# Kernel optimization log

Measured on AMD Instinct MI355X. Metric: run time of the kernel, lower is better.

## Reference

```python
import jax, jax.numpy as jnp
import numpy as np
from jax import lax

B, T = 64, 200
NUM_C, DIM_S, SIZE_M = 2000, 128, 50


def setup_inputs() -> dict:
    key = jax.random.key(0)
    ks = jax.random.split(key, 12)
    d = {}
    d['skill'] = jax.random.randint(ks[0], (B, T), 0, NUM_C)
    d['answer'] = jax.random.randint(ks[1], (B, T), 0, 2)
    s = 1.0 / np.sqrt(DIM_S)
    d['k_emb'] = jax.random.normal(ks[2], (NUM_C + 1, DIM_S), jnp.float32)
    d['v_emb'] = jax.random.normal(ks[3], (2 * NUM_C + 1, DIM_S), jnp.float32)
    # kaiming_normal on [size_m, dim_s]: std = sqrt(2/dim_s)
    d['Mk'] = jax.random.normal(ks[4], (SIZE_M, DIM_S), jnp.float32) * np.sqrt(2.0 / DIM_S)
    d['Mv0'] = jax.random.normal(ks[5], (SIZE_M, DIM_S), jnp.float32) * np.sqrt(2.0 / DIM_S)
    d['f_W'] = jax.random.normal(ks[6], (DIM_S, 2 * DIM_S), jnp.float32) * (1.0 / np.sqrt(2 * DIM_S))
    d['f_b'] = jnp.zeros((DIM_S,), jnp.float32)
    d['p_W'] = jax.random.normal(ks[7], (NUM_C, DIM_S), jnp.float32) * s
    d['p_b'] = jnp.zeros((NUM_C,), jnp.float32)
    d['e_W'] = jax.random.normal(ks[8], (DIM_S, DIM_S), jnp.float32) * s
    d['e_b'] = jnp.zeros((DIM_S,), jnp.float32)
    d['a_W'] = jax.random.normal(ks[9], (DIM_S, DIM_S), jnp.float32) * s
    d['a_b'] = jnp.zeros((DIM_S,), jnp.float32)
    return d


def reference(skill, answer, k_emb, v_emb, Mk, Mv0, f_W, f_b, p_W, p_b, e_W, e_b, a_W, a_b):
    num_c = p_W.shape[0]
    bsz = skill.shape[0]
    answer_x = jnp.where(answer == 2, 1, answer)
    x = skill + num_c * answer_x                       # [B,T]
    k = k_emb[skill]                                   # [B,T,D]
    v = v_emb[x]                                       # [B,T,D]
    w = jax.nn.softmax(jnp.einsum('btd,md->btm', k, Mk), axis=-1)   # [B,T,M]
    e = jax.nn.sigmoid(jnp.einsum('btd,ed->bte', v, e_W) + e_b)      # [B,T,D]
    a = jnp.tanh(jnp.einsum('btd,ed->bte', v, a_W) + a_b)            # [B,T,D]

    Mv_init = jnp.broadcast_to(Mv0, (bsz,) + Mv0.shape)              # [B,M,D]

    def step(Mvt, inp):
        et, at, wt = inp                               # [B,D],[B,D],[B,M]
        # read uses pre-update memory (Mv[:, :-1] in the torch code)
        read = jnp.einsum('bm,bmd->bd', wt, Mvt)
        Mvt_new = Mvt * (1.0 - wt[:, :, None] * et[:, None, :]) + wt[:, :, None] * at[:, None, :]
        return Mvt_new, read

    _, reads = lax.scan(step, Mv_init,
                        (e.transpose(1, 0, 2), a.transpose(1, 0, 2), w.transpose(1, 0, 2)))
    reads = reads.transpose(1, 0, 2)                   # [B,T,D]

    f = jnp.tanh(jnp.concatenate([reads, k], axis=-1) @ f_W.T + f_b)  # [B,T,D]
    p = jax.nn.sigmoid(f @ p_W.T + p_b)                # [B,T,num_c] (dropout is identity at eval)
    p = p[:, :-1, :]
    next_skill = skill[:, 1:]                          # [B,T-1]
    idx = jnp.minimum(next_skill, num_c - 1)
    pred = jnp.take_along_axis(p, idx[..., None], axis=-1)[..., 0]
    pred = jnp.where(next_skill < num_c, pred, 0.0)    # index num_c -> zero row in torch one_hot
    return pred
```

## Files before the change

kernel.cpp:

```cpp
#include <hip/hip_runtime.h>
#include <math.h>

#define Bsz 64
#define Tn 200
#define NUMC 2000
#define DS 128
#define SM 50
#define NTOK (Bsz*Tn)
#define WG2 10
#define MPG2 5

typedef __attribute__((ext_vector_type(8))) short bfrag;
typedef __attribute__((ext_vector_type(4))) float f32x4;
typedef __attribute__((ext_vector_type(4))) unsigned int u32x4;

__device__ __forceinline__ unsigned short f2bf(float x) {
    unsigned int u = __builtin_bit_cast(unsigned int, x);
    u = u + 0x7fffu + ((u >> 16) & 1u);
    return (unsigned short)(u >> 16);
}
__device__ __forceinline__ unsigned int pack2(float a, float b) {
    return (unsigned int)f2bf(a) | ((unsigned int)f2bf(b) << 16);
}
__device__ __forceinline__ bfrag mk_frag(f32x4 x, f32x4 y) {
    u32x4 t;
    t[0] = pack2(x[0], x[1]); t[1] = pack2(x[2], x[3]);
    t[2] = pack2(y[0], y[1]); t[3] = pack2(y[2], y[3]);
    return __builtin_bit_cast(bfrag, t);
}

__device__ __forceinline__ float fast_exp(float x)  { return __builtin_amdgcn_exp2f(x * 1.44269504f); }
__device__ __forceinline__ float fast_rcp(float x)  { return __builtin_amdgcn_rcpf(x); }
__device__ __forceinline__ float fast_sigmoid(float x) { return fast_rcp(1.f + fast_exp(-x)); }
__device__ __forceinline__ float fast_tanh(float x) { return 1.f - 2.f * fast_rcp(fast_exp(2.f * x) + 1.f); }

__device__ __forceinline__ void load_group(const bfrag* __restrict__ B, int nt0, int L, bfrag bf[4][4]) {
    #pragma unroll
    for (int t = 0; t < 4; t++)
        #pragma unroll
        for (int ki = 0; ki < 4; ki++)
            bf[t][ki] = B[(size_t)((nt0 + t) * 4 + ki) * 64 + L];
}
__device__ __forceinline__ void mfma_group(const bfrag A[4], const bfrag bf[4][4], f32x4 acc[4]) {
    #pragma unroll
    for (int ki = 0; ki < 4; ki++)
        #pragma unroll
        for (int t = 0; t < 4; t++)
            acc[t] = __builtin_amdgcn_mfma_f32_16x16x32_bf16(A[ki], bf[t][ki], acc[t], 0, 0, 0);
}

__global__ __launch_bounds__(256) void k0_cast(
    const float* __restrict__ eW, const float* __restrict__ aW,
    const float* __restrict__ fW, const float* __restrict__ Mk,
    unsigned int* __restrict__ BeaU, unsigned int* __restrict__ BkmU,
    unsigned int* __restrict__ Bf0U)
{
    const int g = blockIdx.x * 256 + threadIdx.x;
    if (g >= 9216) return;
    int gm, mat;
    unsigned int* dst;
    if (g < 4096)      { mat = 0; gm = g;        dst = BeaU; }
    else if (g < 7168) { mat = 1; gm = g - 4096; dst = BkmU; }
    else               { mat = 2; gm = g - 7168; dst = Bf0U; }
    const int nt = gm >> 8, r = gm & 255, ki = r >> 6, L = r & 63;
    const int n = nt * 16 + (L & 15);
    const int k = ki * 32 + (L >> 4) * 8;

    const float* src = nullptr;
    if (mat == 0) {
        src = (n < 128) ? (eW + (size_t)n * DS + k) : (aW + (size_t)(n - 128) * DS + k);
    } else if (mat == 1) {
        if (n < 128)      src = fW + (size_t)n * (2 * DS) + DS + k;
        else if (n < 128 + SM) src = Mk + (size_t)(n - 128) * DS + k;
    } else {
        src = fW + (size_t)n * (2 * DS) + k;
    }
    float v[8];
    #pragma unroll
    for (int j = 0; j < 8; j++) v[j] = src ? src[j] : 0.f;
    u32x4 o;
    o[0] = pack2(v[0], v[1]); o[1] = pack2(v[2], v[3]);
    o[2] = pack2(v[4], v[5]); o[3] = pack2(v[6], v[7]);
    ((u32x4*)dst)[gm] = o;
}

__global__ __launch_bounds__(64) void k1_gemm(
    const int* __restrict__ skill, const int* __restrict__ answer,
    const float* __restrict__ k_emb, const float* __restrict__ v_emb,
    const unsigned int* __restrict__ BeaU, const unsigned int* __restrict__ BkmU,
    const float* __restrict__ eB, const float* __restrict__ aB,
    float* __restrict__ w_buf, float* __restrict__ e_buf,
    float* __restrict__ a_buf, float* __restrict__ kp_buf)
{
    const int bid = blockIdx.x;
    const int L = threadIdx.x, L15 = L & 15, quad = L >> 4;

    if (bid < NTOK/16) {
        const int tok0 = bid * 16;
        const int tokA = tok0 + L15;
        const int tokD0 = tok0 + quad * 4;

        const bfrag* Bea = (const bfrag*)BeaU;
        bfrag bfA[4][4], bfB[4][4];
        load_group(Bea, 0, L, bfA);
        load_group(Bea, 4, L, bfB);

        const int s  = skill[tokA];
        const int an = answer[tokA];
        const int ax = (an == 2) ? 1 : an;
        const float* vp = v_emb + ((size_t)(s + NUMC * ax)) * DS + quad * 8;
        bfrag Vf[4];
        #pragma unroll
        for (int ki = 0; ki < 4; ki++) {
            const f32x4* a = (const f32x4*)(vp + ki * 32);
            Vf[ki] = mk_frag(a[0], a[1]);
        }

        f32x4 acc[4];
        #pragma unroll
        for (int t = 0; t < 4; t++) acc[t] = (f32x4){0.f,0.f,0.f,0.f};
        mfma_group(Vf, bfA, acc);
        load_group(Bea, 8, L, bfA);
        #pragma unroll
        for (int t = 0; t < 4; t++) {
            const int n = t * 16 + L15;
            const float bias = eB[n];
            #pragma unroll
            for (int reg = 0; reg < 4; reg++)
                e_buf[(size_t)(tokD0 + reg) * DS + n] = fast_sigmoid(acc[t][reg] + bias);
        }

        #pragma unroll
        for (int t = 0; t < 4; t++) acc[t] = (f32x4){0.f,0.f,0.f,0.f};
        mfma_group(Vf, bfB, acc);
        load_group(Bea, 12, L, bfB);
        #pragma unroll
        for (int t = 0; t < 4; t++) {
            const int n = (4 + t) * 16 + L15;
            const float bias = eB[n];
            #pragma unroll
            for (int reg = 0; reg < 4; reg++)
                e_buf[(size_t)(tokD0 + reg) * DS + n] = fast_sigmoid(acc[t][reg] + bias);
        }

        #pragma unroll
        for (int t = 0; t < 4; t++) acc[t] = (f32x4){0.f,0.f,0.f,0.f};
        mfma_group(Vf, bfA, acc);
        #pragma unroll
        for (int t = 0; t < 4; t++) {
            const int n = t * 16 + L15;
            const float bias = aB[n];
            #pragma unroll
            for (int reg = 0; reg < 4; reg++)
                a_buf[(size_t)(tokD0 + reg) * DS + n] = fast_tanh(acc[t][reg] + bias);
        }

        #pragma unroll
        for (int t = 0; t < 4; t++) acc[t] = (f32x4){0.f,0.f,0.f,0.f};
        mfma_group(Vf, bfB, acc);
        #pragma unroll
        for (int t = 0; t < 4; t++) {
            const int n = (4 + t) * 16 + L15;
            const float bias = aB[n];
            #pragma unroll
            for (int reg = 0; reg < 4; reg++)
                a_buf[(size_t)(tokD0 + reg) * DS + n] = fast_tanh(acc[t][reg] + bias);
        }
    } else {
        const int tok0 = (bid - NTOK/16) * 16;
        const int tokA = tok0 + L15;
        const int tokD0 = tok0 + quad * 4;

        const bfrag* Bkm = (const bfrag*)BkmU;
        bfrag bfA[4][4], bfB[4][4];
        load_group(Bkm, 0, L, bfA);
        load_group(Bkm, 4, L, bfB);

        const int s = skill[tokA];
        const float* kp = k_emb + (size_t)s * DS + quad * 8;
        bfrag Kf[4];
        #pragma unroll
        for (int ki = 0; ki < 4; ki++) {
            const f32x4* b = (const f32x4*)(kp + ki * 32);
            Kf[ki] = mk_frag(b[0], b[1]);
        }

        __shared__ float wl[16][52];

        f32x4 acc[4];
        #pragma unroll
        for (int t = 0; t < 4; t++) acc[t] = (f32x4){0.f,0.f,0.f,0.f};
        mfma_group(Kf, bfA, acc);
        load_group(Bkm, 8, L, bfA);
        #pragma unroll
        for (int t = 0; t < 4; t++) {
            const int n = t * 16 + L15;
            #pragma unroll
            for (int reg = 0; reg < 4; reg++)
                kp_buf[(size_t)(tokD0 + reg) * DS + n] = acc[t][reg];
        }

        #pragma unroll
        for (int t = 0; t < 4; t++) acc[t] = (f32x4){0.f,0.f,0.f,0.f};
        mfma_group(Kf, bfB, acc);
        #pragma unroll
        for (int t = 0; t < 4; t++) {
            const int n = (4 + t) * 16 + L15;
            #pragma unroll
            for (int reg = 0; reg < 4; reg++)
                kp_buf[(size_t)(tokD0 + reg) * DS + n] = acc[t][reg];
        }

        #pragma unroll
        for (int t = 0; t < 4; t++) acc[t] = (f32x4){0.f,0.f,0.f,0.f};
        mfma_group(Kf, bfA, acc);
        #pragma unroll
        for (int t = 0; t < 4; t++) {
            const int c = (8 + t) * 16 + L15 - 128;
            if (c < SM) {
                #pragma unroll
                for (int reg = 0; reg < 4; reg++)
                    wl[quad * 4 + reg][c] = acc[t][reg];
            }
        }
        __syncthreads();
        if (L < 16) {
            float mx = -1e30f;
            for (int m = 0; m < SM; m++) mx = fmaxf(mx, wl[L][m]);
            float sum = 0.f;
            float ex[SM];
            for (int m = 0; m < SM; m++) { ex[m] = fast_exp(wl[L][m] - mx); sum += ex[m]; }
            const float inv = fast_rcp(sum);
            float* wp = w_buf + (size_t)(tok0 + L) * SM;
            for (int m = 0; m < SM; m++) wp[m] = ex[m] * inv;
        }
    }
}

__global__ __launch_bounds__(64) void k2_scan(
    const float* __restrict__ w_buf, const float* __restrict__ e_buf,
    const float* __restrict__ a_buf, const float* __restrict__ Mv0,
    float* __restrict__ part_buf)
{
    const int bi   = blockIdx.x;
    const int b    = bi / (2*WG2);
    const int r    = bi % (2*WG2);
    const int dh   = r / WG2;
    const int mg   = r % WG2;
    const int lane = threadIdx.x;
    const int d    = dh*64 + lane;
    const int m0   = mg * MPG2;
    const int base = b * Tn;

    float Mv[MPG2];
    #pragma unroll
    for (int m = 0; m < MPG2; m++) Mv[m] = Mv0[(size_t)(m0+m)*DS + d];

    float* pout = part_buf + (size_t)mg * NTOK * DS;

    float se[4][2], sa[4][2], sw[4][2][MPG2];

    #define LOADST(ST, T)                                                      \
        { const int tc_ = ((T) < Tn) ? (T) : 0;                                \
          _Pragma("unroll")                                                    \
          for (int q_ = 0; q_ < 2; q_++) {                                     \
              const int tf_ = base + tc_ + q_;                                 \
              se[ST][q_] = e_buf[(size_t)tf_*DS + d];                          \
              sa[ST][q_] = a_buf[(size_t)tf_*DS + d];                          \
              _Pragma("unroll")                                                \
              for (int m_ = 0; m_ < MPG2; m_++)                                \
                  sw[ST][q_][m_] = w_buf[(size_t)tf_*SM + m0 + m_];            \
          } }

    LOADST(0, 0) LOADST(1, 2) LOADST(2, 4) LOADST(3, 6)

    for (int i = 0; i < 25; i++) {
        const int tb = i * 8;
        #pragma unroll
        for (int sub = 0; sub < 4; sub++) {
            const int t0 = tb + sub * 2;
            #pragma unroll
            for (int q = 0; q < 2; q++) {
                const float ev = se[sub][q], av = sa[sub][q];
                float rd = 0.f;
                #pragma unroll
                for (int m = 0; m < MPG2; m++) {
                    const float wm = sw[sub][q][m];
                    rd = fmaf(wm, Mv[m], rd);
                    Mv[m] = fmaf(-wm, fmaf(ev, Mv[m], -av), Mv[m]);
                }
                pout[(size_t)(base + t0 + q)*DS + d] = rd;
            }
            LOADST(sub, t0 + 8)
        }
    }
}

__global__ __launch_bounds__(64) void k3_gemm(
    const float* __restrict__ part_buf, const float* __restrict__ kp_buf,
    const unsigned int* __restrict__ Bf0U, const float* __restrict__ fB,
    const float* __restrict__ pW, const float* __restrict__ pB,
    const int* __restrict__ skill, float* __restrict__ out)
{
    const int L = threadIdx.x, L15 = L & 15, quad = L >> 4;
    const int tok0 = blockIdx.x * 16;
    const int tokA = tok0 + L15;
    const int tokD0 = tok0 + quad * 4;

    const bfrag* Bf0 = (const bfrag*)Bf0U;
    bfrag bfA[4][4], bfB[4][4];
    load_group(Bf0, 0, L, bfA);
    load_group(Bf0, 4, L, bfB);

    bfrag Rf[4];
    #pragma unroll
    for (int ki = 0; ki < 4; ki++) {
        const float* p0 = part_buf + (size_t)tokA * DS + ki * 32 + quad * 8;
        f32x4 x = (f32x4){0.f,0.f,0.f,0.f}, y = (f32x4){0.f,0.f,0.f,0.f};
        #pragma unroll
        for (int g = 0; g < WG2; g++) {
            const f32x4* q4 = (const f32x4*)(p0 + (size_t)g * NTOK * DS);
            x = x + q4[0]; y = y + q4[1];
        }
        Rf[ki] = mk_frag(x, y);
    }

    float f[4][8];
    f32x4 acc[4];

    #pragma unroll
    for (int t = 0; t < 4; t++) acc[t] = (f32x4){0.f,0.f,0.f,0.f};
    mfma_group(Rf, bfA, acc);
    #pragma unroll
    for (int t = 0; t < 4; t++) {
        const int n = t * 16 + L15;
        const float fb = fB[n];
        #pragma unroll
        for (int reg = 0; reg < 4; reg++)
            f[reg][t] = fast_tanh(acc[t][reg] + kp_buf[(size_t)(tokD0 + reg) * DS + n] + fb);
    }

    #pragma unroll
    for (int t = 0; t < 4; t++) acc[t] = (f32x4){0.f,0.f,0.f,0.f};
    mfma_group(Rf, bfB, acc);
    #pragma unroll
    for (int t = 0; t < 4; t++) {
        const int n = (4 + t) * 16 + L15;
        const float fb = fB[n];
        #pragma unroll
        for (int reg = 0; reg < 4; reg++)
            f[reg][4 + t] = fast_tanh(acc[t][reg] + kp_buf[(size_t)(tokD0 + reg) * DS + n] + fb);
    }

    #pragma unroll
    for (int reg = 0; reg < 4; reg++) {
        const int tok = tokD0 + reg;
        const int t = tok % Tn;
        const bool act = (t < Tn - 1);
        int sn = 0, ix = 0;
        float contrib = 0.f;
        if (act) {
            sn = skill[tok + 1];
            ix = (sn < NUMC) ? sn : (NUMC - 1);
            const float* pr = pW + (size_t)ix * DS + L15;
            #pragma unroll
            for (int nt = 0; nt < 8; nt++)
                contrib = fmaf(f[reg][nt], pr[nt * 16], contrib);
        }
        #pragma unroll
        for (int msk = 1; msk <= 8; msk <<= 1)
            contrib += __shfl_xor(contrib, msk);
        if (act && L15 == 0) {
            const float val = contrib + pB[ix];
            const float prd = (sn < NUMC) ? fast_sigmoid(val) : 0.f;
            out[(size_t)(tok / Tn) * (Tn - 1) + t] = prd;
        }
    }
}

extern "C" void kernel_launch(void* const* d_in, const int* in_sizes, int n_in,
                              void* d_out, int out_size, void* d_ws, size_t ws_size,
                              hipStream_t stream)
{
    const int*   skill  = (const int*)  d_in[0];
    const int*   answer = (const int*)  d_in[1];
    const float* k_emb  = (const float*)d_in[2];
    const float* v_emb  = (const float*)d_in[3];
    const float* Mk     = (const float*)d_in[4];
    const float* Mv0    = (const float*)d_in[5];
    const float* f_W    = (const float*)d_in[6];
    const float* f_b    = (const float*)d_in[7];
    const float* p_W    = (const float*)d_in[8];
    const float* p_b    = (const float*)d_in[9];
    const float* e_W    = (const float*)d_in[10];
    const float* e_b    = (const float*)d_in[11];
    const float* a_W    = (const float*)d_in[12];
    const float* a_b    = (const float*)d_in[13];
    float* out = (float*)d_out;

    float* ws       = (float*)d_ws;
    float* w_buf    = ws;
    float* e_buf    = w_buf    + (size_t)NTOK*SM;
    float* a_buf    = e_buf    + (size_t)NTOK*DS;
    float* kp_buf   = a_buf    + (size_t)NTOK*DS;
    float* part_buf = kp_buf   + (size_t)NTOK*DS;
    unsigned int* BeaU = (unsigned int*)(part_buf + (size_t)WG2*NTOK*DS);
    unsigned int* BkmU = BeaU + 4096 * 4;
    unsigned int* Bf0U = BkmU + 3072 * 4;

    k0_cast<<<36, 256, 0, stream>>>(e_W, a_W, f_W, Mk, BeaU, BkmU, Bf0U);
    k1_gemm<<<2*(NTOK/16), 64, 0, stream>>>(skill, answer, k_emb, v_emb,
        BeaU, BkmU, e_b, a_b, w_buf, e_buf, a_buf, kp_buf);
    k2_scan<<<Bsz*2*WG2, 64, 0, stream>>>(w_buf, e_buf, a_buf, Mv0, part_buf);
    k3_gemm<<<NTOK/16, 64, 0, stream>>>(part_buf, kp_buf, Bf0U, f_b,
        p_W, p_b, skill, out);
}
```

Before: 141.9 us.

## Reduce scan memory-slot partials in LDS instead of global partial buffer

The scan kernel now packs the ten memory-slot groups for one (batch, half-dim) into a single 640-thread workgroup. Each group writes its partial read values into a double-buffered LDS array, and after every 8 timesteps the groups are summed and a single reads buffer is written. This removes the 10x partial-sum global writes from the scan and the 10-way global re-read in the GEMM kernel. In exchange it adds a __syncthreads every 8 steps, which couples the ten waves' progress, and it cuts the number of workgroups to 128.

```diff
diff --git a/kernel.cpp b/kernel.cpp
--- a/kernel.cpp
+++ b/kernel.cpp
@@ -237,26 +237,25 @@
     }
 }
 
-__global__ __launch_bounds__(64) void k2_scan(
+__global__ __launch_bounds__(640) void k2_scan(
     const float* __restrict__ w_buf, const float* __restrict__ e_buf,
     const float* __restrict__ a_buf, const float* __restrict__ Mv0,
-    float* __restrict__ part_buf)
+    float* __restrict__ reads_buf)
 {
     const int bi   = blockIdx.x;
-    const int b    = bi / (2*WG2);
-    const int r    = bi % (2*WG2);
-    const int dh   = r / WG2;
-    const int mg   = r % WG2;
-    const int lane = threadIdx.x;
-    const int d    = dh*64 + lane;
-    const int m0   = mg * MPG2;
+    const int b    = bi >> 1;
+    const int dh   = bi & 1;
+    const int wv   = threadIdx.x >> 6;
+    const int lane = threadIdx.x & 63;
+    const int d    = dh * 64 + lane;
+    const int m0   = wv * MPG2;
     const int base = b * Tn;
 
+    __shared__ float red[2][WG2][8][64];
+
     float Mv[MPG2];
     #pragma unroll
     for (int m = 0; m < MPG2; m++) Mv[m] = Mv0[(size_t)(m0+m)*DS + d];
-
-    float* pout = part_buf + (size_t)mg * NTOK * DS;
 
     float se[4][2], sa[4][2], sw[4][2][MPG2];
 
@@ -276,6 +275,7 @@
 
     for (int i = 0; i < 25; i++) {
         const int tb = i * 8;
+        const int p  = i & 1;
         #pragma unroll
         for (int sub = 0; sub < 4; sub++) {
             const int t0 = tb + sub * 2;
@@ -289,15 +289,25 @@
                     rd = fmaf(wm, Mv[m], rd);
                     Mv[m] = fmaf(-wm, fmaf(ev, Mv[m], -av), Mv[m]);
                 }
-                pout[(size_t)(base + t0 + q)*DS + d] = rd;
+                red[p][wv][sub * 2 + q][lane] = rd;
             }
             LOADST(sub, t0 + 8)
         }
-    }
+        __syncthreads();
+        const int j = threadIdx.x;
+        if (j < 512) {
+            const int tt = j >> 6, dd = j & 63;
+            float s = red[p][0][tt][dd];
+            #pragma unroll
+            for (int g = 1; g < WG2; g++) s += red[p][g][tt][dd];
+            reads_buf[(size_t)(base + tb + tt) * DS + dh * 64 + dd] = s;
+        }
+    }
+    #undef LOADST
 }
 
 __global__ __launch_bounds__(64) void k3_gemm(
-    const float* __restrict__ part_buf, const float* __restrict__ kp_buf,
+    const float* __restrict__ reads_buf, const float* __restrict__ kp_buf,
     const unsigned int* __restrict__ Bf0U, const float* __restrict__ fB,
     const float* __restrict__ pW, const float* __restrict__ pB,
     const int* __restrict__ skill, float* __restrict__ out)
@@ -315,14 +325,8 @@
     bfrag Rf[4];
     #pragma unroll
     for (int ki = 0; ki < 4; ki++) {
-        const float* p0 = part_buf + (size_t)tokA * DS + ki * 32 + quad * 8;
-        f32x4 x = (f32x4){0.f,0.f,0.f,0.f}, y = (f32x4){0.f,0.f,0.f,0.f};
-        #pragma unroll
-        for (int g = 0; g < WG2; g++) {
-            const f32x4* q4 = (const f32x4*)(p0 + (size_t)g * NTOK * DS);
-            x = x + q4[0]; y = y + q4[1];
-        }
-        Rf[ki] = mk_frag(x, y);
+        const f32x4* q4 = (const f32x4*)(reads_buf + (size_t)tokA * DS + ki * 32 + quad * 8);
+        Rf[ki] = mk_frag(q4[0], q4[1]);
     }
 
     float f[4][8];
@@ -398,20 +402,20 @@
     const float* a_b    = (const float*)d_in[13];
     float* out = (float*)d_out;
 
-    float* ws       = (float*)d_ws;
-    float* w_buf    = ws;
-    float* e_buf    = w_buf    + (size_t)NTOK*SM;
-    float* a_buf    = e_buf    + (size_t)NTOK*DS;
-    float* kp_buf   = a_buf    + (size_t)NTOK*DS;
-    float* part_buf = kp_buf   + (size_t)NTOK*DS;
-    unsigned int* BeaU = (unsigned int*)(part_buf + (size_t)WG2*NTOK*DS);
+    float* ws        = (float*)d_ws;
+    float* w_buf     = ws;
+    float* e_buf     = w_buf     + (size_t)NTOK*SM;
+    float* a_buf     = e_buf     + (size_t)NTOK*DS;
+    float* kp_buf    = a_buf     + (size_t)NTOK*DS;
+    float* reads_buf = kp_buf    + (size_t)NTOK*DS;
+    unsigned int* BeaU = (unsigned int*)(reads_buf + (size_t)NTOK*DS);
     unsigned int* BkmU = BeaU + 4096 * 4;
     unsigned int* Bf0U = BkmU + 3072 * 4;
 
     k0_cast<<<36, 256, 0, stream>>>(e_W, a_W, f_W, Mk, BeaU, BkmU, Bf0U);
     k1_gemm<<<2*(NTOK/16), 64, 0, stream>>>(skill, answer, k_emb, v_emb,
         BeaU, BkmU, e_b, a_b, w_buf, e_buf, a_buf, kp_buf);
-    k2_scan<<<Bsz*2*WG2, 64, 0, stream>>>(w_buf, e_buf, a_buf, Mv0, part_buf);
-    k3_gemm<<<NTOK/16, 64, 0, stream>>>(part_buf, kp_buf, Bf0U, f_b,
+    k2_scan<<<Bsz*2, 640, 0, stream>>>(w_buf, e_buf, a_buf, Mv0, reads_buf);
+    k3_gemm<<<NTOK/16, 64, 0, stream>>>(reads_buf, kp_buf, Bf0U, f_b,
         p_W, p_b, skill, out);
 }
```

Result: no change. 144.2 us (+1.6%).

## Split projection GEMMs into per-role blocks, widen scan split, add separate reduction

Applied to the files above, without the earlier changes.

The projection kernel now launches seven single-wave blocks per 16-token tile, one per output slice (e, a, kp halves, and the softmax weights). The softmax becomes a shuffle-based reduction in registers instead of going through shared memory. The scan splits memory slots into 25 groups of 2 rather than 10 groups of 5, which gives more parallel blocks but more partial buffers. A new reduction kernel sums those partials into bf16 reads, and the final GEMM uses two waves per tile. The aim is higher occupancy and parallelism, in exchange for more partial-sum traffic and an extra launch.

```diff
diff --git a/kernel.cpp b/kernel.cpp
--- a/kernel.cpp
+++ b/kernel.cpp
@@ -7,12 +7,13 @@
 #define DS 128
 #define SM 50
 #define NTOK (Bsz*Tn)
-#define WG2 10
-#define MPG2 5
+#define WG2 25
+#define MPG2 2
 
 typedef __attribute__((ext_vector_type(8))) short bfrag;
 typedef __attribute__((ext_vector_type(4))) float f32x4;
 typedef __attribute__((ext_vector_type(4))) unsigned int u32x4;
+typedef __attribute__((ext_vector_type(2))) unsigned int u32x2;
 
 __device__ __forceinline__ unsigned short f2bf(float x) {
     unsigned int u = __builtin_bit_cast(unsigned int, x);
@@ -33,21 +34,6 @@
 __device__ __forceinline__ float fast_rcp(float x)  { return __builtin_amdgcn_rcpf(x); }
 __device__ __forceinline__ float fast_sigmoid(float x) { return fast_rcp(1.f + fast_exp(-x)); }
 __device__ __forceinline__ float fast_tanh(float x) { return 1.f - 2.f * fast_rcp(fast_exp(2.f * x) + 1.f); }
-
-__device__ __forceinline__ void load_group(const bfrag* __restrict__ B, int nt0, int L, bfrag bf[4][4]) {
-    #pragma unroll
-    for (int t = 0; t < 4; t++)
-        #pragma unroll
-        for (int ki = 0; ki < 4; ki++)
-            bf[t][ki] = B[(size_t)((nt0 + t) * 4 + ki) * 64 + L];
-}
-__device__ __forceinline__ void mfma_group(const bfrag A[4], const bfrag bf[4][4], f32x4 acc[4]) {
-    #pragma unroll
-    for (int ki = 0; ki < 4; ki++)
-        #pragma unroll
-        for (int t = 0; t < 4; t++)
-            acc[t] = __builtin_amdgcn_mfma_f32_16x16x32_bf16(A[ki], bf[t][ki], acc[t], 0, 0, 0);
-}
 
 __global__ __launch_bounds__(256) void k0_cast(
     const float* __restrict__ eW, const float* __restrict__ aW,
@@ -84,7 +70,7 @@
     ((u32x4*)dst)[gm] = o;
 }
 
-__global__ __launch_bounds__(64) void k1_gemm(
+__global__ __launch_bounds__(64, 4) void k1_gemm(
     const int* __restrict__ skill, const int* __restrict__ answer,
     const float* __restrict__ k_emb, const float* __restrict__ v_emb,
     const unsigned int* __restrict__ BeaU, const unsigned int* __restrict__ BkmU,
@@ -93,151 +79,93 @@
     float* __restrict__ a_buf, float* __restrict__ kp_buf)
 {
     const int bid = blockIdx.x;
+    const int tile = bid / 7, role = bid % 7;
     const int L = threadIdx.x, L15 = L & 15, quad = L >> 4;
-
-    if (bid < NTOK/16) {
-        const int tok0 = bid * 16;
-        const int tokA = tok0 + L15;
-        const int tokD0 = tok0 + quad * 4;
-
-        const bfrag* Bea = (const bfrag*)BeaU;
-        bfrag bfA[4][4], bfB[4][4];
-        load_group(Bea, 0, L, bfA);
-        load_group(Bea, 4, L, bfB);
-
-        const int s  = skill[tokA];
+    const int tok0 = tile * 16;
+    const int tokA = tok0 + L15;
+    const int row0 = tok0 + quad * 4;
+
+    const int s = skill[tokA];
+    const float* ap;
+    if (role < 4) {
         const int an = answer[tokA];
         const int ax = (an == 2) ? 1 : an;
-        const float* vp = v_emb + ((size_t)(s + NUMC * ax)) * DS + quad * 8;
-        bfrag Vf[4];
-        #pragma unroll
-        for (int ki = 0; ki < 4; ki++) {
-            const f32x4* a = (const f32x4*)(vp + ki * 32);
-            Vf[ki] = mk_frag(a[0], a[1]);
-        }
-
-        f32x4 acc[4];
-        #pragma unroll
-        for (int t = 0; t < 4; t++) acc[t] = (f32x4){0.f,0.f,0.f,0.f};
-        mfma_group(Vf, bfA, acc);
-        load_group(Bea, 8, L, bfA);
+        ap = v_emb + ((size_t)(s + NUMC * ax)) * DS + quad * 8;
+    } else {
+        ap = k_emb + (size_t)s * DS + quad * 8;
+    }
+    bfrag Af[4];
+    #pragma unroll
+    for (int ki = 0; ki < 4; ki++) {
+        const f32x4* a4 = (const f32x4*)(ap + ki * 32);
+        Af[ki] = mk_frag(a4[0], a4[1]);
+    }
+
+    const bfrag* Bp = (role < 4) ? (const bfrag*)BeaU : (const bfrag*)BkmU;
+    const int g0 = (role < 4) ? role * 4 : (role - 4) * 4;
+
+    f32x4 acc[4];
+    #pragma unroll
+    for (int t = 0; t < 4; t++) acc[t] = (f32x4){0.f,0.f,0.f,0.f};
+
+    #pragma unroll
+    for (int half = 0; half < 2; half++) {
+        bfrag bh[2][4];
+        #pragma unroll
+        for (int tt = 0; tt < 2; tt++)
+            #pragma unroll
+            for (int ki = 0; ki < 4; ki++)
+                bh[tt][ki] = Bp[(size_t)((g0 + half * 2 + tt) * 4 + ki) * 64 + L];
+        #pragma unroll
+        for (int ki = 0; ki < 4; ki++)
+            #pragma unroll
+            for (int tt = 0; tt < 2; tt++)
+                acc[half * 2 + tt] = __builtin_amdgcn_mfma_f32_16x16x32_bf16(
+                    Af[ki], bh[tt][ki], acc[half * 2 + tt], 0, 0, 0);
+    }
+
+    if (role == 6) {
+        #pragma unroll
+        for (int reg = 0; reg < 4; reg++) {
+            float mx = -1e30f;
+            #pragma unroll
+            for (int t = 0; t < 4; t++) { const int c = t * 16 + L15; if (c < SM) mx = fmaxf(mx, acc[t][reg]); }
+            #pragma unroll
+            for (int msk = 1; msk <= 8; msk <<= 1) mx = fmaxf(mx, __shfl_xor(mx, msk));
+            float ex[4]; float ssum = 0.f;
+            #pragma unroll
+            for (int t = 0; t < 4; t++) {
+                const int c = t * 16 + L15;
+                ex[t] = (c < SM) ? fast_exp(acc[t][reg] - mx) : 0.f;
+                ssum += ex[t];
+            }
+            #pragma unroll
+            for (int msk = 1; msk <= 8; msk <<= 1) ssum += __shfl_xor(ssum, msk);
+            const float inv = fast_rcp(ssum);
+            float* wp = w_buf + (size_t)(row0 + reg) * SM;
+            #pragma unroll
+            for (int t = 0; t < 4; t++) { const int c = t * 16 + L15; if (c < SM) wp[c] = ex[t] * inv; }
+        }
+    } else {
+        const int nb = (role & 1) * 64;
+        float* obuf = (role < 2) ? e_buf : (role < 4) ? a_buf : kp_buf;
+        const float* bias = (role < 2) ? eB : aB;
         #pragma unroll
         for (int t = 0; t < 4; t++) {
-            const int n = t * 16 + L15;
-            const float bias = eB[n];
-            #pragma unroll
-            for (int reg = 0; reg < 4; reg++)
-                e_buf[(size_t)(tokD0 + reg) * DS + n] = fast_sigmoid(acc[t][reg] + bias);
-        }
-
-        #pragma unroll
-        for (int t = 0; t < 4; t++) acc[t] = (f32x4){0.f,0.f,0.f,0.f};
-        mfma_group(Vf, bfB, acc);
-        load_group(Bea, 12, L, bfB);
-        #pragma unroll
-        for (int t = 0; t < 4; t++) {
-            const int n = (4 + t) * 16 + L15;
-            const float bias = eB[n];
-            #pragma unroll
-            for (int reg = 0; reg < 4; reg++)
-                e_buf[(size_t)(tokD0 + reg) * DS + n] = fast_sigmoid(acc[t][reg] + bias);
-        }
-
-        #pragma unroll
-        for (int t = 0; t < 4; t++) acc[t] = (f32x4){0.f,0.f,0.f,0.f};
-        mfma_group(Vf, bfA, acc);
-        #pragma unroll
-        for (int t = 0; t < 4; t++) {
-            const int n = t * 16 + L15;
-            const float bias = aB[n];
-            #pragma unroll
-            for (int reg = 0; reg < 4; reg++)
-                a_buf[(size_t)(tokD0 + reg) * DS + n] = fast_tanh(acc[t][reg] + bias);
-        }
-
-        #pragma unroll
-        for (int t = 0; t < 4; t++) acc[t] = (f32x4){0.f,0.f,0.f,0.f};
-        mfma_group(Vf, bfB, acc);
-        #pragma unroll
-        for (int t = 0; t < 4; t++) {
-            const int n = (4 + t) * 16 + L15;
-            const float bias = aB[n];
-            #pragma unroll
-            for (int reg = 0; reg < 4; reg++)
-                a_buf[(size_t)(tokD0 + reg) * DS + n] = fast_tanh(acc[t][reg] + bias);
-        }
-    } else {
-        const int tok0 = (bid - NTOK/16) * 16;
-        const int tokA = tok0 + L15;
-        const int tokD0 = tok0 + quad * 4;
-
-        const bfrag* Bkm = (const bfrag*)BkmU;
-        bfrag bfA[4][4], bfB[4][4];
-        load_group(Bkm, 0, L, bfA);
-        load_group(Bkm, 4, L, bfB);
-
-        const int s = skill[tokA];
-        const float* kp = k_emb + (size_t)s * DS + quad * 8;
-        bfrag Kf[4];
-        #pragma unroll
-        for (int ki = 0; ki < 4; ki++) {
-            const f32x4* b = (const f32x4*)(kp + ki * 32);
-            Kf[ki] = mk_frag(b[0], b[1]);
-        }
-
-        __shared__ float wl[16][52];
-
-        f32x4 acc[4];
-        #pragma unroll
-        for (int t = 0; t < 4; t++) acc[t] = (f32x4){0.f,0.f,0.f,0.f};
-        mfma_group(Kf, bfA, acc);
-        load_group(Bkm, 8, L, bfA);
-        #pragma unroll
-        for (int t = 0; t < 4; t++) {
-            const int n = t * 16 + L15;
-            #pragma unroll
-            for (int reg = 0; reg < 4; reg++)
-                kp_buf[(size_t)(tokD0 + reg) * DS + n] = acc[t][reg];
-        }
-
-        #pragma unroll
-        for (int t = 0; t < 4; t++) acc[t] = (f32x4){0.f,0.f,0.f,0.f};
-        mfma_group(Kf, bfB, acc);
-        #pragma unroll
-        for (int t = 0; t < 4; t++) {
-            const int n = (4 + t) * 16 + L15;
-            #pragma unroll
-            for (int reg = 0; reg < 4; reg++)
-                kp_buf[(size_t)(tokD0 + reg) * DS + n] = acc[t][reg];
-        }
-
-        #pragma unroll
-        for (int t = 0; t < 4; t++) acc[t] = (f32x4){0.f,0.f,0.f,0.f};
-        mfma_group(Kf, bfA, acc);
-        #pragma unroll
-        for (int t = 0; t < 4; t++) {
-            const int c = (8 + t) * 16 + L15 - 128;
-            if (c < SM) {
-                #pragma unroll
-                for (int reg = 0; reg < 4; reg++)
-                    wl[quad * 4 + reg][c] = acc[t][reg];
+            const int n = nb + t * 16 + L15;
+            const float bv = (role < 4) ? bias[n] : 0.f;
+            #pragma unroll
+            for (int reg = 0; reg < 4; reg++) {
+                float v = acc[t][reg] + bv;
+                if (role < 2)      v = fast_sigmoid(v);
+                else if (role < 4) v = fast_tanh(v);
+                obuf[(size_t)(row0 + reg) * DS + n] = v;
             }
         }
-        __syncthreads();
-        if (L < 16) {
-            float mx = -1e30f;
-            for (int m = 0; m < SM; m++) mx = fmaxf(mx, wl[L][m]);
-            float sum = 0.f;
-            float ex[SM];
-            for (int m = 0; m < SM; m++) { ex[m] = fast_exp(wl[L][m] - mx); sum += ex[m]; }
-            const float inv = fast_rcp(sum);
-            float* wp = w_buf + (size_t)(tok0 + L) * SM;
-            for (int m = 0; m < SM; m++) wp[m] = ex[m] * inv;
-        }
-    }
-}
-
-__global__ __launch_bounds__(64) void k2_scan(
+    }
+}
+
+__global__ __launch_bounds__(64, 4) void k2_scan(
     const float* __restrict__ w_buf, const float* __restrict__ e_buf,
     const float* __restrict__ a_buf, const float* __restrict__ Mv0,
     float* __restrict__ part_buf)
@@ -294,86 +222,105 @@
             LOADST(sub, t0 + 8)
         }
     }
-}
-
-__global__ __launch_bounds__(64) void k3_gemm(
-    const float* __restrict__ part_buf, const float* __restrict__ kp_buf,
+    #undef LOADST
+}
+
+__global__ __launch_bounds__(256) void k2b_reduce(
+    const float* __restrict__ part_buf, unsigned int* __restrict__ readsU)
+{
+    const int i = blockIdx.x * 256 + threadIdx.x;
+    const f32x4* p = (const f32x4*)part_buf;
+    f32x4 s = p[i];
+    #pragma unroll 4
+    for (int g = 1; g < WG2; g++) s += p[(size_t)g * (NTOK*DS/4) + i];
+    u32x2 o;
+    o[0] = pack2(s[0], s[1]);
+    o[1] = pack2(s[2], s[3]);
+    ((u32x2*)readsU)[i] = o;
+}
+
+__global__ __launch_bounds__(128, 2) void k3_gemm(
+    const unsigned short* __restrict__ reads, const float* __restrict__ kp_buf,
     const unsigned int* __restrict__ Bf0U, const float* __restrict__ fB,
     const float* __restrict__ pW, const float* __restrict__ pB,
     const int* __restrict__ skill, float* __restrict__ out)
 {
-    const int L = threadIdx.x, L15 = L & 15, quad = L >> 4;
+    const int tid = threadIdx.x;
+    const int wv  = tid >> 6;
+    const int L   = tid & 63, L15 = L & 15, quad = L >> 4;
     const int tok0 = blockIdx.x * 16;
     const int tokA = tok0 + L15;
-    const int tokD0 = tok0 + quad * 4;
+    const int row0 = tok0 + quad * 4;
+
+    __shared__ float sm[2][16];
+
+    bfrag Rf[4];
+    #pragma unroll
+    for (int ki = 0; ki < 4; ki++)
+        Rf[ki] = *(const bfrag*)(reads + (size_t)tokA * DS + ki * 32 + quad * 8);
 
     const bfrag* Bf0 = (const bfrag*)Bf0U;
-    bfrag bfA[4][4], bfB[4][4];
-    load_group(Bf0, 0, L, bfA);
-    load_group(Bf0, 4, L, bfB);
-
-    bfrag Rf[4];
-    #pragma unroll
-    for (int ki = 0; ki < 4; ki++) {
-        const float* p0 = part_buf + (size_t)tokA * DS + ki * 32 + quad * 8;
-        f32x4 x = (f32x4){0.f,0.f,0.f,0.f}, y = (f32x4){0.f,0.f,0.f,0.f};
-        #pragma unroll
-        for (int g = 0; g < WG2; g++) {
-            const f32x4* q4 = (const f32x4*)(p0 + (size_t)g * NTOK * DS);
-            x = x + q4[0]; y = y + q4[1];
-        }
-        Rf[ki] = mk_frag(x, y);
-    }
-
-    float f[4][8];
+    const int g0 = wv * 4;
+
     f32x4 acc[4];
-
     #pragma unroll
     for (int t = 0; t < 4; t++) acc[t] = (f32x4){0.f,0.f,0.f,0.f};
-    mfma_group(Rf, bfA, acc);
+
+    #pragma unroll
+    for (int half = 0; half < 2; half++) {
+        bfrag bh[2][4];
+        #pragma unroll
+        for (int tt = 0; tt < 2; tt++)
+            #pragma unroll
+            for (int ki = 0; ki < 4; ki++)
+                bh[tt][ki] = Bf0[(size_t)((g0 + half * 2 + tt) * 4 + ki) * 64 + L];
+        #pragma unroll
+        for (int ki = 0; ki < 4; ki++)
+            #pragma unroll
+            for (int tt = 0; tt < 2; tt++)
+                acc[half * 2 + tt] = __builtin_amdgcn_mfma_f32_16x16x32_bf16(
+                    Rf[ki], bh[tt][ki], acc[half * 2 + tt], 0, 0, 0);
+    }
+
+    const int nb = wv * 64;
+    float f[4][4];
     #pragma unroll
     for (int t = 0; t < 4; t++) {
-        const int n = t * 16 + L15;
+        const int n = nb + t * 16 + L15;
         const float fb = fB[n];
         #pragma unroll
         for (int reg = 0; reg < 4; reg++)
-            f[reg][t] = fast_tanh(acc[t][reg] + kp_buf[(size_t)(tokD0 + reg) * DS + n] + fb);
-    }
-
-    #pragma unroll
-    for (int t = 0; t < 4; t++) acc[t] = (f32x4){0.f,0.f,0.f,0.f};
-    mfma_group(Rf, bfB, acc);
-    #pragma unroll
-    for (int t = 0; t < 4; t++) {
-        const int n = (4 + t) * 16 + L15;
-        const float fb = fB[n];
-        #pragma unroll
-        for (int reg = 0; reg < 4; reg++)
-            f[reg][4 + t] = fast_tanh(acc[t][reg] + kp_buf[(size_t)(tokD0 + reg) * DS + n] + fb);
+            f[reg][t] = fast_tanh(acc[t][reg] + kp_buf[(size_t)(row0 + reg) * DS + n] + fb);
     }
 
     #pragma unroll
     for (int reg = 0; reg < 4; reg++) {
-        const int tok = tokD0 + reg;
+        const int tok = row0 + reg;
         const int t = tok % Tn;
         const bool act = (t < Tn - 1);
-        int sn = 0, ix = 0;
         float contrib = 0.f;
         if (act) {
-            sn = skill[tok + 1];
-            ix = (sn < NUMC) ? sn : (NUMC - 1);
-            const float* pr = pW + (size_t)ix * DS + L15;
-            #pragma unroll
-            for (int nt = 0; nt < 8; nt++)
-                contrib = fmaf(f[reg][nt], pr[nt * 16], contrib);
+            const int sn = skill[tok + 1];
+            const int ix = (sn < NUMC) ? sn : (NUMC - 1);
+            const float* pr = pW + (size_t)ix * DS + nb + L15;
+            #pragma unroll
+            for (int t4 = 0; t4 < 4; t4++)
+                contrib = fmaf(f[reg][t4], pr[t4 * 16], contrib);
         }
         #pragma unroll
         for (int msk = 1; msk <= 8; msk <<= 1)
             contrib += __shfl_xor(contrib, msk);
-        if (act && L15 == 0) {
-            const float val = contrib + pB[ix];
-            const float prd = (sn < NUMC) ? fast_sigmoid(val) : 0.f;
-            out[(size_t)(tok / Tn) * (Tn - 1) + t] = prd;
+        if (L15 == 0) sm[wv][quad * 4 + reg] = contrib;
+    }
+    __syncthreads();
+    if (tid < 16) {
+        const int tok = tok0 + tid;
+        const int t = tok % Tn;
+        if (t < Tn - 1) {
+            const int sn = skill[tok + 1];
+            const int ix = (sn < NUMC) ? sn : (NUMC - 1);
+            const float val = sm[0][tid] + sm[1][tid] + pB[ix];
+            out[(size_t)(tok / Tn) * (Tn - 1) + t] = (sn < NUMC) ? fast_sigmoid(val) : 0.f;
         }
     }
 }
@@ -398,20 +345,22 @@
     const float* a_b    = (const float*)d_in[13];
     float* out = (float*)d_out;
 
-    float* ws       = (float*)d_ws;
-    float* w_buf    = ws;
-    float* e_buf    = w_buf    + (size_t)NTOK*SM;
-    float* a_buf    = e_buf    + (size_t)NTOK*DS;
-    float* kp_buf   = a_buf    + (size_t)NTOK*DS;
-    float* part_buf = kp_buf   + (size_t)NTOK*DS;
-    unsigned int* BeaU = (unsigned int*)(part_buf + (size_t)WG2*NTOK*DS);
+    float* ws     = (float*)d_ws;
+    float* w_buf  = ws;
+    float* e_buf  = w_buf  + (size_t)NTOK*SM;
+    float* a_buf  = e_buf  + (size_t)NTOK*DS;
+    float* kp_buf = a_buf  + (size_t)NTOK*DS;
+    float* part   = kp_buf + (size_t)NTOK*DS;
+    unsigned short* reads = (unsigned short*)(part + (size_t)WG2*NTOK*DS);
+    unsigned int* BeaU = (unsigned int*)(reads + (size_t)NTOK*DS);
     unsigned int* BkmU = BeaU + 4096 * 4;
     unsigned int* Bf0U = BkmU + 3072 * 4;
 
     k0_cast<<<36, 256, 0, stream>>>(e_W, a_W, f_W, Mk, BeaU, BkmU, Bf0U);
-    k1_gemm<<<2*(NTOK/16), 64, 0, stream>>>(skill, answer, k_emb, v_emb,
+    k1_gemm<<<7*(NTOK/16), 64, 0, stream>>>(skill, answer, k_emb, v_emb,
         BeaU, BkmU, e_b, a_b, w_buf, e_buf, a_buf, kp_buf);
-    k2_scan<<<Bsz*2*WG2, 64, 0, stream>>>(w_buf, e_buf, a_buf, Mv0, part_buf);
-    k3_gemm<<<NTOK/16, 64, 0, stream>>>(part_buf, kp_buf, Bf0U, f_b,
+    k2_scan<<<Bsz*2*WG2, 64, 0, stream>>>(w_buf, e_buf, a_buf, Mv0, part);
+    k2b_reduce<<<(NTOK*DS/4)/256, 256, 0, stream>>>(part, (unsigned int*)reads);
+    k3_gemm<<<NTOK/16, 128, 0, stream>>>(reads, kp_buf, Bf0U, f_b,
         p_W, p_b, skill, out);
 }
```

After: 173.0 us. 21.9% more time.
